# Optimization experiments

Hardware: AMD Instinct MI355X
Metric: run time of the kernel (lower is better)

Reference implementation:

```python
import jax, jax.numpy as jnp
import numpy as np

B, IN, OUT = 1024, 512, 512


def setup_inputs() -> dict:
    key = jax.random.key(0)
    kx, kw = jax.random.split(key)
    x = jax.random.normal(kx, (B, IN), dtype=jnp.float32)
    # kaiming_uniform_(a=sqrt(5)) on a (OUT, IN+1) matrix -> U(-bound, bound)
    gain = float(np.sqrt(2.0 / (1.0 + 5.0)))
    bound = gain * float(np.sqrt(3.0 / (IN + 1)))
    weight = jax.random.uniform(kw, (OUT, IN + 1), dtype=jnp.float32,
                                minval=-bound, maxval=bound)
    # fixed frequency ramp: arange(1..OUT) * 2pi/OUT, tiled across IN+1 cols
    w = (jnp.arange(1, OUT + 1, dtype=jnp.float32)[:, None]
         * (2.0 * np.pi / OUT)) * jnp.ones((1, IN + 1), dtype=jnp.float32)
    return {"x": x, "weight": weight, "w": w}


def reference(x, weight, w):
    # x: [B, IN] -> append bias ones column -> [B, 1, IN+1]
    xb = jnp.concatenate([x, jnp.ones((x.shape[0], 1), x.dtype)], axis=1)
    # y[b,o] = sum_i weight[o,i] * sin(w[o,i] * xb[b,i])
    y = jnp.sum(weight[None, :, :] * jnp.sin(w[None, :, :] * xb[:, None, :]),
                axis=2)  # [B, OUT]
    return y
```

## Files before the change

### kernel.cpp

```cpp
#include <hip/hip_runtime.h>


#define B_TOT 1024
#define IN_D  512
#define OUT_D 512
#define LDW   513
#define O_T   16
#define WAVES 8
#define IQ    (IN_D / WAVES)

__global__ __launch_bounds__(256)
void xpose_kernel(const float* __restrict__ x, float* __restrict__ xT)
{
    __shared__ float t[64][65];
    const int i0 = blockIdx.x * 64;
    const int b0 = blockIdx.y * 64;
    const int c  = threadIdx.x & 63;
    const int r0 = threadIdx.x >> 6;
#pragma unroll
    for (int rr = 0; rr < 64; rr += 4) {
        const int r = rr + r0;
        t[r][c] = x[(size_t)(b0 + r) * IN_D + i0 + c];
    }
    __syncthreads();
#pragma unroll
    for (int rr = 0; rr < 64; rr += 4) {
        const int r = rr + r0;
        xT[(size_t)(i0 + r) * B_TOT + b0 + c] = t[c][r];
    }
}

template <bool XT>
__global__ __launch_bounds__(512, 4)
void skan_kernel(const float* __restrict__ x,
                 const float* __restrict__ weight,
                 const float* __restrict__ w,
                 float* __restrict__ out)
{
    __shared__ float red[WAVES][64][O_T + 1];

    const int tid  = threadIdx.x;
    const int lane = tid & 63;
    const int b0   = blockIdx.y * 64;
    const int o0   = blockIdx.x * O_T;
    const int iq   = __builtin_amdgcn_readfirstlane(tid >> 6);
    const int i0   = iq * IQ;

    const float inv2pi = 0.15915493667125702f;
    const float g1    = w[(size_t)o0 * LDW] * inv2pi;
    const float delta = w[(size_t)(o0 + 1) * LDW] * inv2pi - g1;
    const float gp    = g1 - delta;

    const float* __restrict__ wbase = weight + (size_t)o0 * LDW + i0;

    const float* __restrict__ xc   = x + (size_t)i0 * B_TOT + b0 + lane;
    const float* __restrict__ xrow = x + (size_t)(b0 + lane) * IN_D + i0;

    float acc[O_T];
#pragma unroll
    for (int k = 0; k < O_T; ++k) acc[k] = 0.0f;

    float nx[4];
#pragma unroll
    for (int j = 0; j < 4; ++j)
        nx[j] = XT ? xc[(size_t)j * B_TOT] : xrow[j];

    for (int ii = 0; ii < IQ; ii += 4) {
        float xk[4];
#pragma unroll
        for (int j = 0; j < 4; ++j) xk[j] = nx[j];
        if (ii + 4 < IQ) {
#pragma unroll
            for (int j = 0; j < 4; ++j)
                nx[j] = XT ? xc[(size_t)(ii + 4 + j) * B_TOT]
                           : xrow[ii + 4 + j];
        }

        float4 wt[O_T];
#pragma unroll
        for (int k = 0; k < O_T; ++k)
            wt[k] = *reinterpret_cast<const float4*>(wbase + k * LDW + ii);

#pragma unroll
        for (int j = 0; j < 4; ++j) {
            const float xv  = xk[j];
            const float dx  = delta * xv;
            const float c   = __builtin_amdgcn_cosf(dx);
            const float c2  = c + c;
            float sc = __builtin_amdgcn_sinf(g1 * xv);
            float sp = __builtin_amdgcn_sinf(gp * xv);
            const float* wj = &wt[0].x + j;
            acc[0] = fmaf(wj[0], sc, acc[0]);
#pragma unroll
            for (int k = 1; k < O_T; ++k) {
                const float sn = fmaf(c2, sc, -sp);
                acc[k] = fmaf(wj[4 * k], sn, acc[k]);
                sp = sc; sc = sn;
            }
        }
    }

#pragma unroll
    for (int k = 0; k < O_T; ++k) red[iq][lane][k] = acc[k];
    __syncthreads();

    {
        const int b  = tid & 63;
        const int k2 = tid >> 6;
        float2 res;
        float* rp = &res.x;
#pragma unroll
        for (int kk = 0; kk < 2; ++kk) {
            const int k = k2 * 2 + kk;
            float s = 0.0f;
#pragma unroll
            for (int p = 0; p < WAVES; ++p) s += red[p][b][k];
            const int o = o0 + k;
            const float gb = w[(size_t)o * LDW + IN_D] * inv2pi;
            s = fmaf(weight[(size_t)o * LDW + IN_D],
                     __builtin_amdgcn_sinf(gb), s);
            rp[kk] = s;
        }
        *reinterpret_cast<float2*>(
            out + (size_t)(b0 + b) * OUT_D + o0 + k2 * 2) = res;
    }
}

extern "C" void kernel_launch(void* const* d_in, const int* in_sizes, int n_in,
                              void* d_out, int out_size, void* d_ws, size_t ws_size,
                              hipStream_t stream) {
    const float* x      = (const float*)d_in[0];
    const float* weight = (const float*)d_in[1];
    const float* w      = (const float*)d_in[2];
    float* out          = (float*)d_out;

    dim3 grid(OUT_D / O_T, B_TOT / 64);

    if (ws_size >= (size_t)IN_D * B_TOT * sizeof(float)) {
        float* xT = (float*)d_ws;
        dim3 tg(IN_D / 64, B_TOT / 64);
        xpose_kernel<<<tg, 256, 0, stream>>>(x, xT);
        skan_kernel<true><<<grid, 512, 0, stream>>>(xT, weight, w, out);
    } else {
        skan_kernel<false><<<grid, 512, 0, stream>>>(x, weight, w, out);
    }
}
```

Measured before the change: 29.94 us.

## Double output tile per block, split weight loads into halves, stagger wave starts

Raises the output-neuron tile from 16 to 32 so each x value's sin/cos seeds are reused across twice as many outputs through the Chebyshev recurrence. Weights are loaded in two 16-row halves to limit register pressure, and the recurrence state is carried between the halves. Waves are staggered with s_sleep, the x prefetch is removed, and occupancy is lowered to 2 blocks per CU. Fewer blocks are launched, the LDS reduction buffer doubles, and the final store is widened to float4.

Result: slower. 40.31 us (+34.6%).

```diff
diff --git a/kernel.cpp b/kernel.cpp
--- a/kernel.cpp
+++ b/kernel.cpp
@@ -5,7 +5,8 @@
 #define IN_D  512
 #define OUT_D 512
 #define LDW   513
-#define O_T   16
+#define O_T   32
+#define HALF  16
 #define WAVES 8
 #define IQ    (IN_D / WAVES)
 
@@ -31,7 +32,7 @@
 }
 
 template <bool XT>
-__global__ __launch_bounds__(512, 4)
+__global__ __launch_bounds__(512, 2)
 void skan_kernel(const float* __restrict__ x,
                  const float* __restrict__ weight,
                  const float* __restrict__ w,
@@ -45,6 +46,8 @@
     const int o0   = blockIdx.x * O_T;
     const int iq   = __builtin_amdgcn_readfirstlane(tid >> 6);
     const int i0   = iq * IQ;
+
+    for (int t = 0; t < iq; ++t) __builtin_amdgcn_s_sleep(2);
 
     const float inv2pi = 0.15915493667125702f;
     const float g1    = w[(size_t)o0 * LDW] * inv2pi;
@@ -60,41 +63,51 @@
 #pragma unroll
     for (int k = 0; k < O_T; ++k) acc[k] = 0.0f;
 
-    float nx[4];
-#pragma unroll
-    for (int j = 0; j < 4; ++j)
-        nx[j] = XT ? xc[(size_t)j * B_TOT] : xrow[j];
-
     for (int ii = 0; ii < IQ; ii += 4) {
         float xk[4];
 #pragma unroll
-        for (int j = 0; j < 4; ++j) xk[j] = nx[j];
-        if (ii + 4 < IQ) {
+        for (int j = 0; j < 4; ++j)
+            xk[j] = XT ? xc[(size_t)(ii + j) * B_TOT] : xrow[ii + j];
+
+        float4 wt[HALF];
 #pragma unroll
-            for (int j = 0; j < 4; ++j)
-                nx[j] = XT ? xc[(size_t)(ii + 4 + j) * B_TOT]
-                           : xrow[ii + 4 + j];
-        }
-
-        float4 wt[O_T];
-#pragma unroll
-        for (int k = 0; k < O_T; ++k)
+        for (int k = 0; k < HALF; ++k)
             wt[k] = *reinterpret_cast<const float4*>(wbase + k * LDW + ii);
 
+        float c2v[4], spv[4], scv[4];
 #pragma unroll
         for (int j = 0; j < 4; ++j) {
             const float xv  = xk[j];
-            const float dx  = delta * xv;
-            const float c   = __builtin_amdgcn_cosf(dx);
-            const float c2  = c + c;
+            const float dxv = delta * xv;
+            const float cv  = __builtin_amdgcn_cosf(dxv);
+            const float c2  = cv + cv;
             float sc = __builtin_amdgcn_sinf(g1 * xv);
             float sp = __builtin_amdgcn_sinf(gp * xv);
             const float* wj = &wt[0].x + j;
             acc[0] = fmaf(wj[0], sc, acc[0]);
 #pragma unroll
-            for (int k = 1; k < O_T; ++k) {
+            for (int k = 1; k < HALF; ++k) {
                 const float sn = fmaf(c2, sc, -sp);
                 acc[k] = fmaf(wj[4 * k], sn, acc[k]);
+                sp = sc; sc = sn;
+            }
+            c2v[j] = c2; spv[j] = sp; scv[j] = sc;
+        }
+
+#pragma unroll
+        for (int k = 0; k < HALF; ++k)
+            wt[k] = *reinterpret_cast<const float4*>(
+                        wbase + (HALF + k) * LDW + ii);
+
+#pragma unroll
+        for (int j = 0; j < 4; ++j) {
+            const float c2 = c2v[j];
+            float sp = spv[j], sc = scv[j];
+            const float* wj = &wt[0].x + j;
+#pragma unroll
+            for (int k = 0; k < HALF; ++k) {
+                const float sn = fmaf(c2, sc, -sp);
+                acc[HALF + k] = fmaf(wj[4 * k], sn, acc[HALF + k]);
                 sp = sc; sc = sn;
             }
         }
@@ -106,12 +119,12 @@
 
     {
         const int b  = tid & 63;
-        const int k2 = tid >> 6;
-        float2 res;
+        const int k4 = tid >> 6;
+        float4 res;
         float* rp = &res.x;
 #pragma unroll
-        for (int kk = 0; kk < 2; ++kk) {
-            const int k = k2 * 2 + kk;
+        for (int kk = 0; kk < 4; ++kk) {
+            const int k = k4 * 4 + kk;
             float s = 0.0f;
 #pragma unroll
             for (int p = 0; p < WAVES; ++p) s += red[p][b][k];
@@ -121,8 +134,8 @@
                      __builtin_amdgcn_sinf(gb), s);
             rp[kk] = s;
         }
-        *reinterpret_cast<float2*>(
-            out + (size_t)(b0 + b) * OUT_D + o0 + k2 * 2) = res;
+        *reinterpret_cast<float4*>(
+            out + (size_t)(b0 + b) * OUT_D + o0 + k4 * 4) = res;
     }
 }
 
```

## Use stride-2 Chebyshev recurrence on packed float pairs with transposed weights

Applied to the files above, without the earlier changes.

The per-output sine recurrence is restructured to advance two output channels at once using cos(2·delta·x), so packed v2f FMAs (v_pk_fma_f32) can do both lanes of the recurrence and the accumulation. A pre-pass kernel transposes the weight matrix into the workspace so each input column's 16 weights load as one contiguous 64-byte vector instead of 16 strided float4 loads. The changes aim to halve the dependent recurrence chain and the VALU instruction count, and to simplify weight loads. The cost is an extra kernel launch plus transposing 1 MB of weights on every call, one more sine evaluation per input, and a larger workspace requirement.

Result: slower. 34.06 us (+13.8%).

```diff
diff --git a/kernel.cpp b/kernel.cpp
--- a/kernel.cpp
+++ b/kernel.cpp
@@ -6,8 +6,12 @@
 #define OUT_D 512
 #define LDW   513
 #define O_T   16
+#define NPAIR (O_T / 2)
 #define WAVES 8
 #define IQ    (IN_D / WAVES)
+
+typedef float v2f  __attribute__((ext_vector_type(2)));
+typedef float v16f __attribute__((ext_vector_type(16)));
 
 __global__ __launch_bounds__(256)
 void xpose_kernel(const float* __restrict__ x, float* __restrict__ xT)
@@ -30,11 +34,33 @@
     }
 }
 
-template <bool XT>
+__global__ __launch_bounds__(256)
+void wpose_kernel(const float* __restrict__ wsrc, float* __restrict__ wT2)
+{
+    __shared__ float t[64][65];
+    const int i0 = blockIdx.x * 64;
+    const int o0 = blockIdx.y * 64;
+    const int c  = threadIdx.x & 63;
+    const int r0 = threadIdx.x >> 6;
+#pragma unroll
+    for (int rr = 0; rr < 64; rr += 4) {
+        const int r = rr + r0;
+        t[r][c] = wsrc[(size_t)(o0 + r) * LDW + i0 + c];
+    }
+    __syncthreads();
+#pragma unroll
+    for (int rr = 0; rr < 64; rr += 4) {
+        const int r = rr + r0;
+        wT2[(size_t)(i0 + r) * OUT_D + o0 + c] = t[c][r];
+    }
+}
+
+template <bool FAST>
 __global__ __launch_bounds__(512, 4)
 void skan_kernel(const float* __restrict__ x,
                  const float* __restrict__ weight,
                  const float* __restrict__ w,
+                 const float* __restrict__ wT2,
                  float* __restrict__ out)
 {
     __shared__ float red[WAVES][64][O_T + 1];
@@ -49,21 +75,20 @@
     const float inv2pi = 0.15915493667125702f;
     const float g1    = w[(size_t)o0 * LDW] * inv2pi;
     const float delta = w[(size_t)(o0 + 1) * LDW] * inv2pi - g1;
-    const float gp    = g1 - delta;
-
-    const float* __restrict__ wbase = weight + (size_t)o0 * LDW + i0;
+    const float gm1   = g1 - delta;
+    const float gp1   = g1 + delta;
 
     const float* __restrict__ xc   = x + (size_t)i0 * B_TOT + b0 + lane;
     const float* __restrict__ xrow = x + (size_t)(b0 + lane) * IN_D + i0;
 
-    float acc[O_T];
-#pragma unroll
-    for (int k = 0; k < O_T; ++k) acc[k] = 0.0f;
+    v2f acc[NPAIR];
+#pragma unroll
+    for (int m = 0; m < NPAIR; ++m) acc[m] = (v2f)0.0f;
 
     float nx[4];
 #pragma unroll
     for (int j = 0; j < 4; ++j)
-        nx[j] = XT ? xc[(size_t)j * B_TOT] : xrow[j];
+        nx[j] = FAST ? xc[(size_t)j * B_TOT] : xrow[j];
 
     for (int ii = 0; ii < IQ; ii += 4) {
         float xk[4];
@@ -72,36 +97,63 @@
         if (ii + 4 < IQ) {
 #pragma unroll
             for (int j = 0; j < 4; ++j)
-                nx[j] = XT ? xc[(size_t)(ii + 4 + j) * B_TOT]
-                           : xrow[ii + 4 + j];
-        }
-
+                nx[j] = FAST ? xc[(size_t)(ii + 4 + j) * B_TOT]
+                             : xrow[ii + 4 + j];
+        }
+
+        v16f wv[4];
         float4 wt[O_T];
-#pragma unroll
-        for (int k = 0; k < O_T; ++k)
-            wt[k] = *reinterpret_cast<const float4*>(wbase + k * LDW + ii);
+        if (FAST) {
+#pragma unroll
+            for (int j = 0; j < 4; ++j)
+                wv[j] = *reinterpret_cast<const v16f*>(
+                            wT2 + (size_t)(i0 + ii + j) * OUT_D + o0);
+        } else {
+#pragma unroll
+            for (int k = 0; k < O_T; ++k)
+                wt[k] = *reinterpret_cast<const float4*>(
+                            weight + (size_t)(o0 + k) * LDW + i0 + ii);
+        }
 
 #pragma unroll
         for (int j = 0; j < 4; ++j) {
-            const float xv  = xk[j];
+            const float xv = xk[j];
             const float dx  = delta * xv;
-            const float c   = __builtin_amdgcn_cosf(dx);
-            const float c2  = c + c;
-            float sc = __builtin_amdgcn_sinf(g1 * xv);
-            float sp = __builtin_amdgcn_sinf(gp * xv);
-            const float* wj = &wt[0].x + j;
-            acc[0] = fmaf(wj[0], sc, acc[0]);
-#pragma unroll
-            for (int k = 1; k < O_T; ++k) {
-                const float sn = fmaf(c2, sc, -sp);
-                acc[k] = fmaf(wj[4 * k], sn, acc[k]);
-                sp = sc; sc = sn;
+            const float c1  = __builtin_amdgcn_cosf(dx);
+            const float c21 = c1 + c1;
+            const float C2  = fmaf(c21, c21, -2.0f);
+            const float sm1 = __builtin_amdgcn_sinf(gm1 * xv);
+            const float s0  = __builtin_amdgcn_sinf(g1  * xv);
+            const float s1  = __builtin_amdgcn_sinf(gp1 * xv);
+            const float sm2 = fmaf(c21, sm1, -s0);
+            v2f P  = {s0, s1};
+            v2f Pm = {sm2, sm1};
+            const v2f C2v = {C2, C2};
+
+            const v2f* wp = FAST
+                ? reinterpret_cast<const v2f*>(&wv[j]) : nullptr;
+
+            {
+                const v2f w0 = FAST ? wp[0]
+                    : (v2f){(&wt[0].x)[j], (&wt[1].x)[j]};
+                acc[0] = __builtin_elementwise_fma(w0, P, acc[0]);
             }
-        }
-    }
-
-#pragma unroll
-    for (int k = 0; k < O_T; ++k) red[iq][lane][k] = acc[k];
+#pragma unroll
+            for (int m = 1; m < NPAIR; ++m) {
+                const v2f Pn = __builtin_elementwise_fma(C2v, P, -Pm);
+                const v2f wm = FAST ? wp[m]
+                    : (v2f){(&wt[2 * m].x)[j], (&wt[2 * m + 1].x)[j]};
+                acc[m] = __builtin_elementwise_fma(wm, Pn, acc[m]);
+                Pm = P; P = Pn;
+            }
+        }
+    }
+
+#pragma unroll
+    for (int m = 0; m < NPAIR; ++m) {
+        red[iq][lane][2 * m]     = acc[m].x;
+        red[iq][lane][2 * m + 1] = acc[m].y;
+    }
     __syncthreads();
 
     {
@@ -136,12 +188,18 @@
 
     dim3 grid(OUT_D / O_T, B_TOT / 64);
 
-    if (ws_size >= (size_t)IN_D * B_TOT * sizeof(float)) {
-        float* xT = (float*)d_ws;
+    const size_t wT2_bytes = (size_t)IN_D * OUT_D * sizeof(float);
+    const size_t xT_bytes  = (size_t)IN_D * B_TOT * sizeof(float);
+
+    if (ws_size >= wT2_bytes + xT_bytes) {
+        float* wT2 = (float*)d_ws;
+        float* xT  = (float*)((char*)d_ws + wT2_bytes);
+        dim3 wg(IN_D / 64, OUT_D / 64);
         dim3 tg(IN_D / 64, B_TOT / 64);
+        wpose_kernel<<<wg, 256, 0, stream>>>(weight, wT2);
         xpose_kernel<<<tg, 256, 0, stream>>>(x, xT);
-        skan_kernel<true><<<grid, 512, 0, stream>>>(xT, weight, w, out);
+        skan_kernel<true><<<grid, 512, 0, stream>>>(xT, weight, w, wT2, out);
     } else {
-        skan_kernel<false><<<grid, 512, 0, stream>>>(x, weight, w, out);
-    }
-}
+        skan_kernel<false><<<grid, 512, 0, stream>>>(x, weight, w, nullptr, out);
+    }
+}
```
